# Kernel optimization log

Hardware: AMD Instinct MI355X
Metric: run time of the kernel (lower is better)

The kernel has to match this reference:

```python
import jax, jax.numpy as jnp
import numpy as np

D_MODEL = 512
H = 8
D_K = D_MODEL // H


def setup_inputs() -> dict:
    key = jax.random.key(0)
    ks = jax.random.split(key, 11)
    B, S = 2, 2048
    scale = 1.0 / np.sqrt(D_MODEL)
    return {
        "q": jax.random.normal(ks[0], (B, S, D_MODEL), jnp.float32),
        "v": jax.random.normal(ks[1], (B, S, D_MODEL), jnp.float32),
        "k": jax.random.normal(ks[2], (B, S, D_MODEL), jnp.float32),
        "w_q": jax.random.normal(ks[3], (D_MODEL, D_MODEL), jnp.float32) * scale,
        "b_q": jnp.zeros((D_MODEL,), jnp.float32),
        "w_k": jax.random.normal(ks[4], (D_MODEL, D_MODEL), jnp.float32) * scale,
        "b_k": jnp.zeros((D_MODEL,), jnp.float32),
        "w_v": jax.random.normal(ks[5], (D_MODEL, D_MODEL), jnp.float32) * scale,
        "b_v": jnp.zeros((D_MODEL,), jnp.float32),
        "w_o": jax.random.normal(ks[6], (D_MODEL, D_MODEL), jnp.float32) * scale,
        "b_o": jnp.zeros((D_MODEL,), jnp.float32),
    }


def reference(q, v, k, w_q, b_q, w_k, b_k, w_v, b_v, w_o, b_o):
    B, S, _ = q.shape
    # projections (nn.Linear: x @ W.T + b)
    query = q @ w_q.T + b_q
    key_t = k @ w_k.T + b_k
    value = v @ w_v.T + b_v
    # split heads: [B, S, H, D_K] -> [B, H, S, D_K]
    query = query.reshape(B, S, H, D_K).transpose(0, 2, 1, 3)
    key_t = key_t.reshape(B, S, H, D_K).transpose(0, 2, 1, 3)
    value = value.reshape(B, S, H, D_K).transpose(0, 2, 1, 3)
    # unfused attention: full [B, H, S, S] score matrix
    scores = jnp.einsum("bhqd,bhkd->bhqk", query, key_t) / jnp.sqrt(
        jnp.asarray(D_K, query.dtype)
    )
    attn = jax.nn.softmax(scores, axis=-1)  # dropout inactive in eval
    x = jnp.einsum("bhqk,bhkd->bhqd", attn, value)
    # merge heads and output projection
    x = x.transpose(0, 2, 1, 3).reshape(B, S, D_MODEL)
    return x @ w_o.T + b_o
```

## Files before the change

### kernel.cpp

```cpp
#include <hip/hip_runtime.h>
#include <hip/hip_bf16.h>


typedef __attribute__((ext_vector_type(8))) short short8;
typedef __attribute__((ext_vector_type(4))) short short4v;
typedef __attribute__((ext_vector_type(4))) float f32x4;
typedef __attribute__((ext_vector_type(2))) unsigned int uint2v;

#define DM 512
#define SEQ 2048
#define NROW 4096
#define LOG2E 1.44269504088896341f
#define MFMA(a, b, c) __builtin_amdgcn_mfma_f32_16x16x32_bf16(a, b, c, 0, 0, 0)
#define FENCE() __asm__ __volatile__("" ::: "memory")

#if __has_builtin(__builtin_amdgcn_exp2f)
#define EXP2(x) __builtin_amdgcn_exp2f(x)
#else
#define EXP2(x) exp2f(x)
#endif

__device__ __forceinline__ float bf_bits2f(short s) {
    unsigned int u = ((unsigned int)(unsigned short)s) << 16;
    return __builtin_bit_cast(float, u);
}
__device__ __forceinline__ short f2bf_r(float f) {
    unsigned int u = __builtin_bit_cast(unsigned int, f) + 0x8000u;
    return (short)(u >> 16);
}
__device__ __forceinline__ unsigned int pack_bf16(float lo, float hi) {
    unsigned int ul = __builtin_bit_cast(unsigned int, lo) + 0x8000u;
    unsigned int uh = __builtin_bit_cast(unsigned int, hi) + 0x8000u;
    return __builtin_amdgcn_perm(uh, ul, 0x07060302u);
}

__device__ __forceinline__ void gload_lds16(const void* src, void* lds_dst) {
    __builtin_amdgcn_global_load_lds(
        (const __attribute__((address_space(1))) unsigned int*)src,
        (__attribute__((address_space(3))) unsigned int*)lds_dst, 16, 0, 0);
}

template <int ROWS, int NW>
__device__ __forceinline__ void stage_tile(const short* __restrict__ gsrc, size_t gstride,
                                           short* lds, int wave, int lane) {
    constexpr int ISSUES = ROWS * 8 / (64 * NW);
    #pragma unroll
    for (int i = 0; i < ISSUES; i++) {
        const int blk = i * NW + wave;
        const int g = blk * 64 + lane;
        const int row = g >> 3;
        const int cb = (g & 7) ^ (row & 7);
        gload_lds16(gsrc + (size_t)row * gstride + cb * 8, lds + (size_t)blk * 512);
    }
}

__device__ __forceinline__ bool detect_f32(const unsigned int* __restrict__ q, int* cnt_lds) {
    if (threadIdx.x == 0) *cnt_lds = 0;
    __syncthreads();
    int local = 0;
    for (int i = threadIdx.x; i < 1024; i += blockDim.x) {
        unsigned int lo = q[i] & 0x7FFFu;
        if (lo >= 0x3000u && lo < 0x4400u) local++;
    }
    if (local) atomicAdd(cnt_lds, local);
    __syncthreads();
    return *cnt_lds < 512;
}

struct ConvArgs { const void* src[11]; short* dst[11]; int n[11]; };
__global__ void convert_all(ConvArgs a) {
    __shared__ int cnt;
    const bool f32m = detect_f32((const unsigned int*)a.src[0], &cnt);
    const int tid = blockIdx.x * 256 + threadIdx.x;
    const int stride = gridDim.x * 256;
    if (f32m) {
        for (int s = 0; s < 11; s++) {
            const float4* sp = (const float4*)a.src[s];
            short4v* dp = (short4v*)a.dst[s];
            const int n4 = a.n[s] >> 2;
            for (int i = tid; i < n4; i += stride) {
                float4 v = sp[i];
                short4v o;
                o[0] = f2bf_r(v.x); o[1] = f2bf_r(v.y);
                o[2] = f2bf_r(v.z); o[3] = f2bf_r(v.w);
                dp[i] = o;
            }
        }
    } else {
        for (int s = 0; s < 11; s++) {
            const short4v* sp = (const short4v*)a.src[s];
            short4v* dp = (short4v*)a.dst[s];
            const int n4 = a.n[s] >> 2;
            for (int i = tid; i < n4; i += stride) dp[i] = sp[i];
        }
    }
}

template <int MT>
__device__ __forceinline__ void gemm_core(const short* __restrict__ A,
                                          const short* __restrict__ W,
                                          int m0, int n0, short* Alds, short* Blds,
                                          int wave, int lane, f32x4 (&acc)[MT / 64][4]) {
    const int rc = lane & 15, quad = lane >> 4;
    const short* Ag = A + (size_t)m0 * DM;
    const short* Bg = W + (size_t)n0 * DM;
    constexpr int ABUF = MT * 64, BBUF = 64 * 64;
    constexpr int INFLIGHT = MT * 8 / 256 + 2;
    constexpr int NITER = DM / 64;

    stage_tile<MT, 4>(Ag, DM, Alds, wave, lane);
    stage_tile<64, 4>(Bg, DM, Blds, wave, lane);

    for (int i = 0; i < NITER; i++) {
        const int cur = i & 1;
        const short* Ac = Alds + cur * ABUF;
        const short* Bc = Blds + cur * BBUF;
        if (i + 1 < NITER) {
            stage_tile<MT, 4>(Ag + (i + 1) * 64, DM, Alds + (cur ^ 1) * ABUF, wave, lane);
            stage_tile<64, 4>(Bg + (i + 1) * 64, DM, Blds + (cur ^ 1) * BBUF, wave, lane);
            __builtin_amdgcn_s_waitcnt(0x3F70 | INFLIGHT);
        } else {
            __builtin_amdgcn_s_waitcnt(0x3F70);
        }
        FENCE();
        __builtin_amdgcn_s_barrier();
        FENCE();
        #pragma unroll
        for (int h = 0; h < 2; h++) {
            short8 bf[4];
            #pragma unroll
            for (int nt = 0; nt < 4; nt++) {
                const int br = nt * 16 + rc;
                bf[nt] = *(const short8*)&Bc[br * 64 + (((quad + 4 * h) ^ (br & 7)) * 8)];
            }
            #pragma unroll
            for (int ms = 0; ms < MT / 64; ms++) {
                const int ar = wave * (MT / 4) + ms * 16 + rc;
                short8 af = *(const short8*)&Ac[ar * 64 + (((quad + 4 * h) ^ (ar & 7)) * 8)];
                #pragma unroll
                for (int nt = 0; nt < 4; nt++)
                    acc[ms][nt] = MFMA(af, bf[nt], acc[ms][nt]);
            }
        }
        FENCE();
        __builtin_amdgcn_s_barrier();
        FENCE();
    }
}

struct QKVArgs {
    const short* A[3]; const short* W[3]; const short* Bi[3];
    short* Cq; short* Ck; short* Cv;
};
__global__ __launch_bounds__(256, 3) void qkv_gemm(QKVArgs args) {
    __shared__ __align__(16) short Alds[2][128 * 64];
    __shared__ __align__(16) short Blds[2][64 * 64];
    const int z = blockIdx.z;
    const int wave = threadIdx.x >> 6, lane = threadIdx.x & 63;
    const int rc = lane & 15, quad = lane >> 4;
    const int m0 = blockIdx.x * 128, n0 = blockIdx.y * 64;

    f32x4 acc[2][4] = {};
    gemm_core<128>(args.A[z], args.W[z], m0, n0, &Alds[0][0], &Blds[0][0], wave, lane, acc);
    const short* bias = args.Bi[z];

    if (z == 2) {
        const int hh = n0 >> 6;
        #pragma unroll
        for (int ms = 0; ms < 2; ms++) {
            const int mw = m0 + wave * 32 + ms * 16;
            const int b = mw >> 11, sb = (mw & 2047) + quad * 4;
            #pragma unroll
            for (int nt = 0; nt < 4; nt++) {
                const int d = nt * 16 + rc;
                const float bv = bf_bits2f(bias[n0 + d]);
                short4v pk;
                #pragma unroll
                for (int r = 0; r < 4; r++) pk[r] = f2bf_r(acc[ms][nt][r] + bv);
                *(short4v*)(args.Cv + ((size_t)((b * 8 + hh) * 64 + d)) * SEQ + sb) = pk;
            }
        }
    } else {
        short* C = (z == 0) ? args.Cq : args.Ck;
        const float sc = (z == 0) ? (0.125f * LOG2E) : 1.0f;
        #pragma unroll
        for (int ms = 0; ms < 2; ms++) {
            const int mw = m0 + wave * 32 + ms * 16;
            #pragma unroll
            for (int nt = 0; nt < 4; nt++) {
                const int col = n0 + nt * 16 + rc;
                const float bv = bf_bits2f(bias[col]);
                #pragma unroll
                for (int r = 0; r < 4; r++)
                    C[(size_t)(mw + quad * 4 + r) * DM + col] = f2bf_r((acc[ms][nt][r] + bv) * sc);
            }
        }
    }
}

__global__ __launch_bounds__(256, 4) void out_gemm(
    const short* __restrict__ A, const short* __restrict__ W,
    const short* __restrict__ bias, void* __restrict__ Cout,
    const unsigned int* __restrict__ qraw) {
    __shared__ __align__(16) short Alds[2][64 * 64];
    __shared__ __align__(16) short Blds[2][64 * 64];
    __shared__ int cnt;
    const bool f32out = detect_f32(qraw, &cnt);
    const int wave = threadIdx.x >> 6, lane = threadIdx.x & 63;
    const int rc = lane & 15, quad = lane >> 4;
    const int m0 = blockIdx.x * 64, n0 = blockIdx.y * 64;
    f32x4 acc[1][4] = {};
    gemm_core<64>(A, W, m0, n0, &Alds[0][0], &Blds[0][0], wave, lane, acc);
    const int mw = m0 + wave * 16;
    #pragma unroll
    for (int nt = 0; nt < 4; nt++) {
        const int col = n0 + nt * 16 + rc;
        const float bv = bf_bits2f(bias[col]);
        #pragma unroll
        for (int r = 0; r < 4; r++) {
            const size_t idx = (size_t)(mw + quad * 4 + r) * DM + col;
            const float val = acc[0][nt][r] + bv;
            if (f32out) ((float*)Cout)[idx] = val;
            else        ((short*)Cout)[idx] = f2bf_r(val);
        }
    }
}

__global__ __launch_bounds__(256, 2) void attn_kernel(
    const short* __restrict__ Q, const short* __restrict__ K,
    const short* __restrict__ Vt, short* __restrict__ X)
{
    __shared__ __align__(16) short Klds[2][64 * 64];
    __shared__ __align__(16) short Vlds[2][64 * 64];
    __shared__ __align__(16) short Plds[4][16 * 72];

    const int wave = threadIdx.x >> 6, lane = threadIdx.x & 63;
    const int rc = lane & 15, quad = lane >> 4;
    const int L = blockIdx.x;
    const int bh = (L & 7) * 2 + ((L >> 3) >> 5);
    const int qb = (L >> 3) & 31;
    const size_t baseQK = (size_t)(bh >> 3) * SEQ * DM + (size_t)(bh & 7) * 64;
    const short* Qb = Q + baseQK;
    const short* Kb = K + baseQK;
    const short* Vb = Vt + (size_t)bh * 64 * SEQ;
    const int q0 = qb * 64 + wave * 16;

    short8 qa[2];
    #pragma unroll
    for (int h = 0; h < 2; h++)
        qa[h] = *(const short8*)(Qb + (size_t)(q0 + rc) * DM + h * 32 + quad * 8);

    short8 ones;
    #pragma unroll
    for (int j = 0; j < 8; j++) ones[j] = (short)0x3F80;

    f32x4 o[4] = {};
    f32x4 lsum = {};
    short* Pw = &Plds[wave][0];

    int koff[4][2], voff[4][2];
    #pragma unroll
    for (int kt = 0; kt < 4; kt++) {
        const int row = rc * 4 + kt;
        #pragma unroll
        for (int h = 0; h < 2; h++)
            koff[kt][h] = row * 64 + (((quad + 4 * h) ^ (row & 7)) * 8);
    }
    #pragma unroll
    for (int dt = 0; dt < 4; dt++) {
        const int row = dt * 16 + rc;
        #pragma unroll
        for (int h = 0; h < 2; h++)
            voff[dt][h] = row * 64 + (((quad + 4 * h) ^ (row & 7)) * 8);
    }

    stage_tile<64, 4>(Kb, DM, &Klds[0][0], wave, lane);
    stage_tile<64, 4>(Vb, SEQ, &Vlds[0][0], wave, lane);

    auto body = [&](int it, int cur) {
        if (it + 1 < 32) {
            const int k0n = (it + 1) * 64;
            stage_tile<64, 4>(Kb + (size_t)k0n * DM, DM, &Klds[cur ^ 1][0], wave, lane);
            stage_tile<64, 4>(Vb + k0n, SEQ, &Vlds[cur ^ 1][0], wave, lane);
            __builtin_amdgcn_s_waitcnt(0x3F74);
        } else {
            __builtin_amdgcn_s_waitcnt(0x3F70);
        }
        FENCE();
        __builtin_amdgcn_s_barrier();
        FENCE();

        const short* Kt = &Klds[cur][0];
        const short* Vl = &Vlds[cur][0];

        short8 kf[4][2];
        #pragma unroll
        for (int kt = 0; kt < 4; kt++)
            #pragma unroll
            for (int h = 0; h < 2; h++)
                kf[kt][h] = *(const short8*)&Kt[koff[kt][h]];
        f32x4 s[4];
        __builtin_amdgcn_s_setprio(1);
        #pragma unroll
        for (int kt = 0; kt < 4; kt++) {
            f32x4 t = {};
            t = MFMA(qa[0], kf[kt][0], t);
            t = MFMA(qa[1], kf[kt][1], t);
            s[kt] = t;
        }
        __builtin_amdgcn_s_setprio(0);
        #pragma unroll
        for (int r = 0; r < 4; r++) {
            uint2v pk;
            pk[0] = pack_bf16(EXP2(s[0][r]), EXP2(s[1][r]));
            pk[1] = pack_bf16(EXP2(s[2][r]), EXP2(s[3][r]));
            *(uint2v*)(&Pw[(quad * 4 + r) * 72 + rc * 4]) = pk;
        }
        __builtin_amdgcn_s_waitcnt(0xC07F);
        short8 pa[2];
        #pragma unroll
        for (int h = 0; h < 2; h++)
            pa[h] = *(const short8*)(&Pw[rc * 72 + h * 32 + quad * 8]);
        __builtin_amdgcn_s_setprio(1);
        lsum = MFMA(ones, pa[0], lsum);
        lsum = MFMA(ones, pa[1], lsum);
        #pragma unroll
        for (int dt = 0; dt < 4; dt++) {
            short8 v0 = *(const short8*)&Vl[voff[dt][0]];
            short8 v1 = *(const short8*)&Vl[voff[dt][1]];
            o[dt] = MFMA(v0, pa[0], o[dt]);
            o[dt] = MFMA(v1, pa[1], o[dt]);
        }
        __builtin_amdgcn_s_setprio(0);
        FENCE();
        __builtin_amdgcn_s_barrier();
        FENCE();
    };

    for (int itp = 0; itp < 32; itp += 2) {
        body(itp, 0);
        body(itp + 1, 1);
    }

    const float inv = 1.0f / lsum[0];
    short* Xr = X + baseQK;
    const size_t rowoff = (size_t)(q0 + rc) * DM;
    #pragma unroll
    for (int dt = 0; dt < 4; dt++) {
        short4v pk;
        #pragma unroll
        for (int r = 0; r < 4; r++) pk[r] = f2bf_r(o[dt][r] * inv);
        *(short4v*)(Xr + rowoff + dt * 16 + quad * 4) = pk;
    }
}

extern "C" void kernel_launch(void* const* d_in, const int* in_sizes, int n_in,
                              void* d_out, int out_size, void* d_ws, size_t ws_size,
                              hipStream_t stream) {
    char* ws = (char*)d_ws;
    const size_t SEQB = (size_t)NROW * DM * sizeof(short);
    const size_t WB   = (size_t)DM * DM * sizeof(short);
    const size_t BB   = (size_t)DM * sizeof(short);

    size_t off = 0;
    short* qc = (short*)(ws + off); off += SEQB;
    short* vc = (short*)(ws + off); off += SEQB;
    short* kc = (short*)(ws + off); off += SEQB;
    short* wq = (short*)(ws + off); off += WB;
    short* wk = (short*)(ws + off); off += WB;
    short* wv = (short*)(ws + off); off += WB;
    short* wo = (short*)(ws + off); off += WB;
    short* bq = (short*)(ws + off); off += BB;
    short* bk = (short*)(ws + off); off += BB;
    short* bv = (short*)(ws + off); off += BB;
    short* bo = (short*)(ws + off); off += BB;
    off = (off + 255) & ~(size_t)255;
    short* Qp  = (short*)(ws + off); off += SEQB;
    short* Kp  = (short*)(ws + off); off += SEQB;
    short* Vtp = (short*)(ws + off); off += SEQB;
    short* Xp  = (short*)(ws + off); off += SEQB;

    ConvArgs ca;
    const void* srcs[11] = {d_in[0], d_in[1], d_in[2], d_in[3], d_in[5], d_in[7],
                            d_in[9], d_in[4], d_in[6], d_in[8], d_in[10]};
    short* dsts[11] = {qc, vc, kc, wq, wk, wv, wo, bq, bk, bv, bo};
    int ns[11] = {NROW * DM, NROW * DM, NROW * DM, DM * DM, DM * DM, DM * DM,
                  DM * DM, DM, DM, DM, DM};
    for (int i = 0; i < 11; i++) { ca.src[i] = srcs[i]; ca.dst[i] = dsts[i]; ca.n[i] = ns[i]; }
    convert_all<<<1024, 256, 0, stream>>>(ca);

    QKVArgs qa;
    qa.A[0] = qc; qa.A[1] = kc; qa.A[2] = vc;
    qa.W[0] = wq; qa.W[1] = wk; qa.W[2] = wv;
    qa.Bi[0] = bq; qa.Bi[1] = bk; qa.Bi[2] = bv;
    qa.Cq = Qp; qa.Ck = Kp; qa.Cv = Vtp;
    qkv_gemm<<<dim3(NROW / 128, DM / 64, 3), 256, 0, stream>>>(qa);

    attn_kernel<<<dim3(512), 256, 0, stream>>>(Qp, Kp, Vtp, Xp);

    out_gemm<<<dim3(NROW / 64, DM / 64), 256, 0, stream>>>(
        Xp, wo, bo, d_out, (const unsigned int*)d_in[0]);
}
```

Before: 156.1 us.

## Split attention waves across query and key halves with LDS partial-sum merge

Restructures the attention block so each wave handles 32 query rows and half of a 128-key tile, instead of 16 query rows over a 64-key tile. Each K/V fragment loaded from LDS is now reused for two query subtiles, and the loop runs 16 larger iterations, halving the barrier count. The two key-halves' partial O and row sums are merged through LDS at the end. In exchange the kernel uses more LDS and registers, which may cut occupancy at the declared launch bounds, and it adds an XOR-swizzled P layout plus a final reduction step.

```diff
diff --git a/kernel.cpp b/kernel.cpp
--- a/kernel.cpp
+++ b/kernel.cpp
@@ -230,12 +230,13 @@
     const short* __restrict__ Q, const short* __restrict__ K,
     const short* __restrict__ Vt, short* __restrict__ X)
 {
-    __shared__ __align__(16) short Klds[2][64 * 64];
-    __shared__ __align__(16) short Vlds[2][64 * 64];
-    __shared__ __align__(16) short Plds[4][16 * 72];
+    __shared__ __align__(16) short Klds[2][128 * 64];
+    __shared__ __align__(16) short Vlds[2][2][64 * 64];
+    __shared__ __align__(16) short Plds[4][32 * 64];
 
     const int wave = threadIdx.x >> 6, lane = threadIdx.x & 63;
     const int rc = lane & 15, quad = lane >> 4;
+    const int qh = wave & 1, kh = wave >> 1;
     const int L = blockIdx.x;
     const int bh = (L & 7) * 2 + ((L >> 3) >> 5);
     const int qb = (L >> 3) & 31;
@@ -243,28 +244,30 @@
     const short* Qb = Q + baseQK;
     const short* Kb = K + baseQK;
     const short* Vb = Vt + (size_t)bh * 64 * SEQ;
-    const int q0 = qb * 64 + wave * 16;
-
-    short8 qa[2];
-    #pragma unroll
-    for (int h = 0; h < 2; h++)
-        qa[h] = *(const short8*)(Qb + (size_t)(q0 + rc) * DM + h * 32 + quad * 8);
+    const int q0 = qb * 64 + qh * 32;
+
+    short8 qa[2][2];
+    #pragma unroll
+    for (int ms = 0; ms < 2; ms++)
+        #pragma unroll
+        for (int h = 0; h < 2; h++)
+            qa[ms][h] = *(const short8*)(Qb + (size_t)(q0 + ms * 16 + rc) * DM + h * 32 + quad * 8);
 
     short8 ones;
     #pragma unroll
     for (int j = 0; j < 8; j++) ones[j] = (short)0x3F80;
 
-    f32x4 o[4] = {};
-    f32x4 lsum = {};
+    f32x4 o[4][2] = {};
+    f32x4 lsum[2] = {};
     short* Pw = &Plds[wave][0];
 
-    int koff[4][2], voff[4][2];
+    int koff[4][2], voff[4][2], poff[2][2];
     #pragma unroll
     for (int kt = 0; kt < 4; kt++) {
         const int row = rc * 4 + kt;
         #pragma unroll
         for (int h = 0; h < 2; h++)
-            koff[kt][h] = row * 64 + (((quad + 4 * h) ^ (row & 7)) * 8);
+            koff[kt][h] = (kh * 64 + row) * 64 + (((quad + 4 * h) ^ (row & 7)) * 8);
     }
     #pragma unroll
     for (int dt = 0; dt < 4; dt++) {
@@ -273,25 +276,28 @@
         for (int h = 0; h < 2; h++)
             voff[dt][h] = row * 64 + (((quad + 4 * h) ^ (row & 7)) * 8);
     }
-
-    stage_tile<64, 4>(Kb, DM, &Klds[0][0], wave, lane);
-    stage_tile<64, 4>(Vb, SEQ, &Vlds[0][0], wave, lane);
-
-    auto body = [&](int it, int cur) {
-        if (it + 1 < 32) {
-            const int k0n = (it + 1) * 64;
-            stage_tile<64, 4>(Kb + (size_t)k0n * DM, DM, &Klds[cur ^ 1][0], wave, lane);
-            stage_tile<64, 4>(Vb + k0n, SEQ, &Vlds[cur ^ 1][0], wave, lane);
-            __builtin_amdgcn_s_waitcnt(0x3F74);
-        } else {
-            __builtin_amdgcn_s_waitcnt(0x3F70);
-        }
-        FENCE();
-        __builtin_amdgcn_s_barrier();
-        FENCE();
+    #pragma unroll
+    for (int ms = 0; ms < 2; ms++)
+        #pragma unroll
+        for (int h = 0; h < 2; h++)
+            poff[ms][h] = (ms * 16 + rc) * 64 + ((h * 32 + quad * 8) ^ ((rc & 7) << 3));
+
+    stage_tile<128, 4>(Kb, DM, &Klds[0][0], wave, lane);
+    stage_tile<64, 4>(Vb, SEQ, &Vlds[0][0][0], wave, lane);
+    stage_tile<64, 4>(Vb + 64, SEQ, &Vlds[0][1][0], wave, lane);
+    __syncthreads();
+
+    for (int it = 0; it < 16; ++it) {
+        const int cur = it & 1;
+        if (it + 1 < 16) {
+            const int k0n = (it + 1) * 128;
+            stage_tile<128, 4>(Kb + (size_t)k0n * DM, DM, &Klds[cur ^ 1][0], wave, lane);
+            stage_tile<64, 4>(Vb + k0n, SEQ, &Vlds[cur ^ 1][0][0], wave, lane);
+            stage_tile<64, 4>(Vb + k0n + 64, SEQ, &Vlds[cur ^ 1][1][0], wave, lane);
+        }
 
         const short* Kt = &Klds[cur][0];
-        const short* Vl = &Vlds[cur][0];
+        const short* Vl = &Vlds[cur][kh][0];
 
         short8 kf[4][2];
         #pragma unroll
@@ -299,58 +305,84 @@
             #pragma unroll
             for (int h = 0; h < 2; h++)
                 kf[kt][h] = *(const short8*)&Kt[koff[kt][h]];
-        f32x4 s[4];
+        f32x4 s[2][4];
         __builtin_amdgcn_s_setprio(1);
         #pragma unroll
-        for (int kt = 0; kt < 4; kt++) {
-            f32x4 t = {};
-            t = MFMA(qa[0], kf[kt][0], t);
-            t = MFMA(qa[1], kf[kt][1], t);
-            s[kt] = t;
-        }
+        for (int ms = 0; ms < 2; ms++)
+            #pragma unroll
+            for (int kt = 0; kt < 4; kt++) {
+                f32x4 t = {};
+                t = MFMA(qa[ms][0], kf[kt][0], t);
+                t = MFMA(qa[ms][1], kf[kt][1], t);
+                s[ms][kt] = t;
+            }
         __builtin_amdgcn_s_setprio(0);
         #pragma unroll
-        for (int r = 0; r < 4; r++) {
-            uint2v pk;
-            pk[0] = pack_bf16(EXP2(s[0][r]), EXP2(s[1][r]));
-            pk[1] = pack_bf16(EXP2(s[2][r]), EXP2(s[3][r]));
-            *(uint2v*)(&Pw[(quad * 4 + r) * 72 + rc * 4]) = pk;
-        }
+        for (int ms = 0; ms < 2; ms++)
+            #pragma unroll
+            for (int r = 0; r < 4; r++) {
+                const int row = ms * 16 + quad * 4 + r;
+                uint2v pk;
+                pk[0] = pack_bf16(EXP2(s[ms][0][r]), EXP2(s[ms][1][r]));
+                pk[1] = pack_bf16(EXP2(s[ms][2][r]), EXP2(s[ms][3][r]));
+                *(uint2v*)(&Pw[row * 64 + ((rc * 4) ^ ((row & 7) << 3))]) = pk;
+            }
         __builtin_amdgcn_s_waitcnt(0xC07F);
-        short8 pa[2];
-        #pragma unroll
-        for (int h = 0; h < 2; h++)
-            pa[h] = *(const short8*)(&Pw[rc * 72 + h * 32 + quad * 8]);
+        __builtin_amdgcn_sched_barrier(0);
+        short8 pa[2][2];
+        #pragma unroll
+        for (int ms = 0; ms < 2; ms++)
+            #pragma unroll
+            for (int h = 0; h < 2; h++)
+                pa[ms][h] = *(const short8*)(&Pw[poff[ms][h]]);
         __builtin_amdgcn_s_setprio(1);
-        lsum = MFMA(ones, pa[0], lsum);
-        lsum = MFMA(ones, pa[1], lsum);
+        #pragma unroll
+        for (int ms = 0; ms < 2; ms++) {
+            lsum[ms] = MFMA(ones, pa[ms][0], lsum[ms]);
+            lsum[ms] = MFMA(ones, pa[ms][1], lsum[ms]);
+        }
         #pragma unroll
         for (int dt = 0; dt < 4; dt++) {
             short8 v0 = *(const short8*)&Vl[voff[dt][0]];
             short8 v1 = *(const short8*)&Vl[voff[dt][1]];
-            o[dt] = MFMA(v0, pa[0], o[dt]);
-            o[dt] = MFMA(v1, pa[1], o[dt]);
+            #pragma unroll
+            for (int ms = 0; ms < 2; ms++) {
+                o[dt][ms] = MFMA(v0, pa[ms][0], o[dt][ms]);
+                o[dt][ms] = MFMA(v1, pa[ms][1], o[dt][ms]);
+            }
         }
         __builtin_amdgcn_s_setprio(0);
-        FENCE();
-        __builtin_amdgcn_s_barrier();
-        FENCE();
-    };
-
-    for (int itp = 0; itp < 32; itp += 2) {
-        body(itp, 0);
-        body(itp + 1, 1);
-    }
-
-    const float inv = 1.0f / lsum[0];
-    short* Xr = X + baseQK;
-    const size_t rowoff = (size_t)(q0 + rc) * DM;
-    #pragma unroll
-    for (int dt = 0; dt < 4; dt++) {
-        short4v pk;
-        #pragma unroll
-        for (int r = 0; r < 4; r++) pk[r] = f2bf_r(o[dt][r] * inv);
-        *(short4v*)(Xr + rowoff + dt * 16 + quad * 4) = pk;
+        __syncthreads();
+    }
+
+    float* OM = (float*)&Plds[0][0];
+    float* LM = (float*)&Klds[0][0];
+    if (kh == 1) {
+        #pragma unroll
+        for (int dt = 0; dt < 4; dt++)
+            #pragma unroll
+            for (int ms = 0; ms < 2; ms++)
+                *(f32x4*)&OM[(((dt * 2 + ms) * 2 + qh) * 64 + lane) * 4] = o[dt][ms];
+        #pragma unroll
+        for (int ms = 0; ms < 2; ms++)
+            LM[(qh * 2 + ms) * 64 + lane] = lsum[ms][0];
+    }
+    __syncthreads();
+    if (kh == 0) {
+        short* Xr = X + baseQK;
+        #pragma unroll
+        for (int ms = 0; ms < 2; ms++) {
+            const float inv = 1.0f / (lsum[ms][0] + LM[(qh * 2 + ms) * 64 + lane]);
+            const size_t rowoff = (size_t)(q0 + ms * 16 + rc) * DM;
+            #pragma unroll
+            for (int dt = 0; dt < 4; dt++) {
+                const f32x4 op = *(const f32x4*)&OM[(((dt * 2 + ms) * 2 + qh) * 64 + lane) * 4];
+                short4v pk;
+                #pragma unroll
+                for (int r = 0; r < 4; r++) pk[r] = f2bf_r((o[dt][ms][r] + op[r]) * inv);
+                *(short4v*)(Xr + rowoff + dt * 16 + quad * 4) = pk;
+            }
+        }
     }
 }
 
```

Result: faster. 146.9 us (-5.9%).

## Restructure attention to 8-wave blocks with register K/V loads and shared P tile

Applied to the files above, without the earlier changes.

Rewrites the attention kernel to use 512 threads per block: waves split into two query halves and four key/value slices. K and V fragments are loaded straight from global into registers with prefetch, removing the LDS staging of K/V. P tiles are exchanged through a swizzled shared buffer and partial row sums are reduced across waves at the end. Separately, the output GEMM reads a dtype flag written once by the conversion kernel instead of re-detecting it in every block. The trade-off is more synchronisation per iteration and uncoalesced register loads from global memory.

```diff
diff --git a/kernel.cpp b/kernel.cpp
--- a/kernel.cpp
+++ b/kernel.cpp
@@ -5,7 +5,6 @@
 typedef __attribute__((ext_vector_type(8))) short short8;
 typedef __attribute__((ext_vector_type(4))) short short4v;
 typedef __attribute__((ext_vector_type(4))) float f32x4;
-typedef __attribute__((ext_vector_type(2))) unsigned int uint2v;
 
 #define DM 512
 #define SEQ 2048
@@ -67,10 +66,11 @@
     return *cnt_lds < 512;
 }
 
-struct ConvArgs { const void* src[11]; short* dst[11]; int n[11]; };
+struct ConvArgs { const void* src[11]; short* dst[11]; int n[11]; int* flag; };
 __global__ void convert_all(ConvArgs a) {
     __shared__ int cnt;
     const bool f32m = detect_f32((const unsigned int*)a.src[0], &cnt);
+    if (threadIdx.x == 0) *a.flag = f32m ? 1 : 0;
     const int tid = blockIdx.x * 256 + threadIdx.x;
     const int stride = gridDim.x * 256;
     if (f32m) {
@@ -201,11 +201,10 @@
 __global__ __launch_bounds__(256, 4) void out_gemm(
     const short* __restrict__ A, const short* __restrict__ W,
     const short* __restrict__ bias, void* __restrict__ Cout,
-    const unsigned int* __restrict__ qraw) {
+    const int* __restrict__ dtf) {
     __shared__ __align__(16) short Alds[2][64 * 64];
     __shared__ __align__(16) short Blds[2][64 * 64];
-    __shared__ int cnt;
-    const bool f32out = detect_f32(qraw, &cnt);
+    const bool f32out = (*dtf != 0);
     const int wave = threadIdx.x >> 6, lane = threadIdx.x & 63;
     const int rc = lane & 15, quad = lane >> 4;
     const int m0 = blockIdx.x * 64, n0 = blockIdx.y * 64;
@@ -226,131 +225,131 @@
     }
 }
 
-__global__ __launch_bounds__(256, 2) void attn_kernel(
+__global__ __launch_bounds__(512, 4) void attn_kernel(
     const short* __restrict__ Q, const short* __restrict__ K,
     const short* __restrict__ Vt, short* __restrict__ X)
 {
-    __shared__ __align__(16) short Klds[2][64 * 64];
-    __shared__ __align__(16) short Vlds[2][64 * 64];
-    __shared__ __align__(16) short Plds[4][16 * 72];
+    __shared__ __align__(16) short Plds[2][64 * 128];
 
     const int wave = threadIdx.x >> 6, lane = threadIdx.x & 63;
     const int rc = lane & 15, quad = lane >> 4;
+    const int qh = wave & 1, kv = wave >> 1;
     const int L = blockIdx.x;
-    const int bh = (L & 7) * 2 + ((L >> 3) >> 5);
+    const int bh = (L & 7) * 2 + (L >> 8);
     const int qb = (L >> 3) & 31;
     const size_t baseQK = (size_t)(bh >> 3) * SEQ * DM + (size_t)(bh & 7) * 64;
     const short* Qb = Q + baseQK;
     const short* Kb = K + baseQK;
     const short* Vb = Vt + (size_t)bh * 64 * SEQ;
-    const int q0 = qb * 64 + wave * 16;
-
-    short8 qa[2];
-    #pragma unroll
-    for (int h = 0; h < 2; h++)
-        qa[h] = *(const short8*)(Qb + (size_t)(q0 + rc) * DM + h * 32 + quad * 8);
+    const int q0 = qb * 64 + qh * 32;
+
+    const short* Kl = Kb + (size_t)(kv * 32 + rc * 2) * DM + quad * 8;
+    const short* Vl = Vb + (size_t)(kv * 16 + rc) * SEQ + quad * 8;
+
+    short8 qa[2][2];
+    #pragma unroll
+    for (int ms = 0; ms < 2; ms++)
+        #pragma unroll
+        for (int h = 0; h < 2; h++)
+            qa[ms][h] = *(const short8*)(Qb + (size_t)(q0 + ms * 16 + rc) * DM + h * 32 + quad * 8);
 
     short8 ones;
     #pragma unroll
     for (int j = 0; j < 8; j++) ones[j] = (short)0x3F80;
 
-    f32x4 o[4] = {};
-    f32x4 lsum = {};
-    short* Pw = &Plds[wave][0];
-
-    int koff[4][2], voff[4][2];
-    #pragma unroll
-    for (int kt = 0; kt < 4; kt++) {
-        const int row = rc * 4 + kt;
-        #pragma unroll
-        for (int h = 0; h < 2; h++)
-            koff[kt][h] = row * 64 + (((quad + 4 * h) ^ (row & 7)) * 8);
-    }
-    #pragma unroll
-    for (int dt = 0; dt < 4; dt++) {
-        const int row = dt * 16 + rc;
-        #pragma unroll
-        for (int h = 0; h < 2; h++)
-            voff[dt][h] = row * 64 + (((quad + 4 * h) ^ (row & 7)) * 8);
-    }
-
-    stage_tile<64, 4>(Kb, DM, &Klds[0][0], wave, lane);
-    stage_tile<64, 4>(Vb, SEQ, &Vlds[0][0], wave, lane);
-
-    auto body = [&](int it, int cur) {
-        if (it + 1 < 32) {
-            const int k0n = (it + 1) * 64;
-            stage_tile<64, 4>(Kb + (size_t)k0n * DM, DM, &Klds[cur ^ 1][0], wave, lane);
-            stage_tile<64, 4>(Vb + k0n, SEQ, &Vlds[cur ^ 1][0], wave, lane);
-            __builtin_amdgcn_s_waitcnt(0x3F74);
-        } else {
-            __builtin_amdgcn_s_waitcnt(0x3F70);
-        }
-        FENCE();
-        __builtin_amdgcn_s_barrier();
-        FENCE();
-
-        const short* Kt = &Klds[cur][0];
-        const short* Vl = &Vlds[cur][0];
-
-        short8 kf[4][2];
-        #pragma unroll
-        for (int kt = 0; kt < 4; kt++)
+    f32x4 o[2] = {};
+    f32x4 lsum[2] = {};
+
+    short8 kfA[2][2], kfB[2][2], v[4];
+
+    int pwoff[2][4], proff[2][4];
+    #pragma unroll
+    for (int ms = 0; ms < 2; ms++) {
+        #pragma unroll
+        for (int r = 0; r < 4; r++) {
+            const int row = qh * 32 + ms * 16 + quad * 4 + r;
+            pwoff[ms][r] = row * 128 + ((kv * 32 + rc * 2) ^ ((row & 7) << 3));
+        }
+        const int rrow = qh * 32 + ms * 16 + rc;
+        #pragma unroll
+        for (int c = 0; c < 4; c++)
+            proff[ms][c] = rrow * 128 + ((c * 32 + quad * 8) ^ ((rc & 7) << 3));
+    }
+
+    auto loadK = [&](short8 (&KF)[2][2], int k0) {
+        #pragma unroll
+        for (int kt = 0; kt < 2; kt++)
             #pragma unroll
             for (int h = 0; h < 2; h++)
-                kf[kt][h] = *(const short8*)&Kt[koff[kt][h]];
-        f32x4 s[4];
+                KF[kt][h] = *(const short8*)(Kl + (size_t)(k0 + kt) * DM + h * 32);
+    };
+    auto loadV = [&](int k0) {
+        #pragma unroll
+        for (int c = 0; c < 4; c++)
+            v[c] = *(const short8*)(Vl + k0 + c * 32);
+    };
+
+    loadK(kfA, 0);
+    loadV(0);
+
+    auto body = [&](int it, short8 (&KU)[2][2], short8 (&KL)[2][2]) {
+        short* P = &Plds[it & 1][0];
+        f32x4 s[2][2];
         __builtin_amdgcn_s_setprio(1);
         #pragma unroll
-        for (int kt = 0; kt < 4; kt++) {
-            f32x4 t = {};
-            t = MFMA(qa[0], kf[kt][0], t);
-            t = MFMA(qa[1], kf[kt][1], t);
-            s[kt] = t;
-        }
+        for (int ms = 0; ms < 2; ms++)
+            #pragma unroll
+            for (int kt = 0; kt < 2; kt++) {
+                f32x4 t = {};
+                t = MFMA(qa[ms][0], KU[kt][0], t);
+                t = MFMA(qa[ms][1], KU[kt][1], t);
+                s[ms][kt] = t;
+            }
         __builtin_amdgcn_s_setprio(0);
         #pragma unroll
-        for (int r = 0; r < 4; r++) {
-            uint2v pk;
-            pk[0] = pack_bf16(EXP2(s[0][r]), EXP2(s[1][r]));
-            pk[1] = pack_bf16(EXP2(s[2][r]), EXP2(s[3][r]));
-            *(uint2v*)(&Pw[(quad * 4 + r) * 72 + rc * 4]) = pk;
-        }
-        __builtin_amdgcn_s_waitcnt(0xC07F);
-        short8 pa[2];
-        #pragma unroll
-        for (int h = 0; h < 2; h++)
-            pa[h] = *(const short8*)(&Pw[rc * 72 + h * 32 + quad * 8]);
+        for (int ms = 0; ms < 2; ms++)
+            #pragma unroll
+            for (int r = 0; r < 4; r++)
+                *(unsigned int*)(&P[pwoff[ms][r]]) =
+                    pack_bf16(EXP2(s[ms][0][r]), EXP2(s[ms][1][r]));
+        __syncthreads();
+        if (it + 1 < 16) loadK(KL, (it + 1) * 128);
         __builtin_amdgcn_s_setprio(1);
-        lsum = MFMA(ones, pa[0], lsum);
-        lsum = MFMA(ones, pa[1], lsum);
-        #pragma unroll
-        for (int dt = 0; dt < 4; dt++) {
-            short8 v0 = *(const short8*)&Vl[voff[dt][0]];
-            short8 v1 = *(const short8*)&Vl[voff[dt][1]];
-            o[dt] = MFMA(v0, pa[0], o[dt]);
-            o[dt] = MFMA(v1, pa[1], o[dt]);
+        #pragma unroll
+        for (int c = 0; c < 4; c++) {
+            short8 pa0 = *(const short8*)&P[proff[0][c]];
+            short8 pa1 = *(const short8*)&P[proff[1][c]];
+            if (c == kv) {
+                lsum[0] = MFMA(ones, pa0, lsum[0]);
+                lsum[1] = MFMA(ones, pa1, lsum[1]);
+            }
+            o[0] = MFMA(v[c], pa0, o[0]);
+            o[1] = MFMA(v[c], pa1, o[1]);
         }
         __builtin_amdgcn_s_setprio(0);
-        FENCE();
-        __builtin_amdgcn_s_barrier();
-        FENCE();
+        if (it + 1 < 16) loadV((it + 1) * 128);
     };
 
-    for (int itp = 0; itp < 32; itp += 2) {
-        body(itp, 0);
-        body(itp + 1, 1);
-    }
-
-    const float inv = 1.0f / lsum[0];
+    for (int itp = 0; itp < 16; itp += 2) {
+        body(itp, kfA, kfB);
+        body(itp + 1, kfB, kfA);
+    }
+
+    float* LM = (float*)&Plds[0][0];
+    #pragma unroll
+    for (int ms = 0; ms < 2; ms++)
+        if (quad == 0) LM[kv * 64 + qh * 32 + ms * 16 + rc] = lsum[ms][0];
+    __syncthreads();
     short* Xr = X + baseQK;
-    const size_t rowoff = (size_t)(q0 + rc) * DM;
-    #pragma unroll
-    for (int dt = 0; dt < 4; dt++) {
+    #pragma unroll
+    for (int ms = 0; ms < 2; ms++) {
+        const int qrow = qh * 32 + ms * 16 + rc;
+        const float l = LM[qrow] + LM[64 + qrow] + LM[128 + qrow] + LM[192 + qrow];
+        const float inv = 1.0f / l;
         short4v pk;
         #pragma unroll
-        for (int r = 0; r < 4; r++) pk[r] = f2bf_r(o[dt][r] * inv);
-        *(short4v*)(Xr + rowoff + dt * 16 + quad * 4) = pk;
+        for (int r = 0; r < 4; r++) pk[r] = f2bf_r(o[ms][r] * inv);
+        *(short4v*)(Xr + (size_t)(qb * 64 + qrow) * DM + kv * 16 + quad * 4) = pk;
     }
 }
 
@@ -379,6 +378,7 @@
     short* Kp  = (short*)(ws + off); off += SEQB;
     short* Vtp = (short*)(ws + off); off += SEQB;
     short* Xp  = (short*)(ws + off); off += SEQB;
+    int*   dtf = (int*)(ws + off);  off += 256;
 
     ConvArgs ca;
     const void* srcs[11] = {d_in[0], d_in[1], d_in[2], d_in[3], d_in[5], d_in[7],
@@ -387,6 +387,7 @@
     int ns[11] = {NROW * DM, NROW * DM, NROW * DM, DM * DM, DM * DM, DM * DM,
                   DM * DM, DM, DM, DM, DM};
     for (int i = 0; i < 11; i++) { ca.src[i] = srcs[i]; ca.dst[i] = dsts[i]; ca.n[i] = ns[i]; }
+    ca.flag = dtf;
     convert_all<<<1024, 256, 0, stream>>>(ca);
 
     QKVArgs qa;
@@ -396,8 +397,8 @@
     qa.Cq = Qp; qa.Ck = Kp; qa.Cv = Vtp;
     qkv_gemm<<<dim3(NROW / 128, DM / 64, 3), 256, 0, stream>>>(qa);
 
-    attn_kernel<<<dim3(512), 256, 0, stream>>>(Qp, Kp, Vtp, Xp);
+    attn_kernel<<<dim3(512), 512, 0, stream>>>(Qp, Kp, Vtp, Xp);
 
     out_gemm<<<dim3(NROW / 64, DM / 64), 256, 0, stream>>>(
-        Xp, wo, bo, d_out, (const unsigned int*)d_in[0]);
-}
+        Xp, wo, bo, d_out, dtf);
+}
```

Measured after the change: 176.2 us. 12.9% more time.
